# Optimization experiments

Measured on AMD Instinct MI355X. Metric: run time of the kernel, lower is better.

## Reference

```python
import jax, jax.numpy as jnp
import numpy as np

B, S, D, H = 4, 2048, 1024, 16
DK = D // H

def setup_inputs() -> dict:
    key = jax.random.key(0)
    ks = jax.random.split(key, 5)
    x = jax.random.normal(ks[0], (B, S, D), dtype=jnp.float32)
    scale = 1.0 / np.sqrt(D)
    Wq = jax.random.normal(ks[1], (D, D), dtype=jnp.float32) * scale
    Wk = jax.random.normal(ks[2], (D, D), dtype=jnp.float32) * scale
    Wv = jax.random.normal(ks[3], (D, D), dtype=jnp.float32) * scale
    Wo = jax.random.normal(ks[4], (D, D), dtype=jnp.float32) * scale
    return {"x": x, "Wq": Wq, "Wk": Wk, "Wv": Wv, "Wo": Wo}

def reference(x, Wq, Wk, Wv, Wo):
    # F.linear: y = x @ W.T  (weights stored torch-style [out, in])
    q = jnp.einsum('bsd,ed->bse', x, Wq).reshape(B, S, H, DK).transpose(0, 2, 1, 3)
    k = jnp.einsum('bsd,ed->bse', x, Wk).reshape(B, S, H, DK).transpose(0, 2, 1, 3)
    v = jnp.einsum('bsd,ed->bse', x, Wv).reshape(B, S, H, DK).transpose(0, 2, 1, 3)
    scores = jnp.einsum('bhqd,bhkd->bhqk', q, k) / jnp.sqrt(jnp.float32(DK))
    attn = jax.nn.softmax(scores, axis=-1)  # dropout p=0.0 -> identity
    out = jnp.einsum('bhqk,bhkd->bhqd', attn, v)
    out = out.transpose(0, 2, 1, 3).reshape(B, S, D)
    return jnp.einsum('bsd,ed->bse', out, Wo)
```

## Files before the change

### kernel.cpp

```cpp
#include <hip/hip_runtime.h>
#include <hip/hip_bf16.h>

#define B_ 4
#define S_ 2048
#define D_ 1024
#define H_ 16
#define DK_ 64

typedef __attribute__((ext_vector_type(8))) short short8;
typedef __attribute__((ext_vector_type(4))) float floatx4;
typedef __attribute__((ext_vector_type(16))) float floatx16;
typedef __attribute__((ext_vector_type(4))) unsigned int uint4v;

#define QSCL 0.1803368801111204f

static __device__ __forceinline__ unsigned short f2bf(float f) {
    unsigned int u = __float_as_uint(f);
    u += 0x7fffu + ((u >> 16) & 1u);
    return (unsigned short)(u >> 16);
}

static __device__ __forceinline__ unsigned int pack2bf_perm(float a, float b) {
    unsigned int u0 = __float_as_uint(a) + 0x8000u;
    unsigned int u1 = __float_as_uint(b) + 0x8000u;
    return __builtin_amdgcn_perm(u1, u0, 0x07060302u);
}

static __device__ __forceinline__ unsigned int pack2bf(float a, float b) {
    return (unsigned int)f2bf(a) | ((unsigned int)f2bf(b) << 16);
}

#define PLSWAP(a, b) asm volatile("v_permlane32_swap_b32 %0, %1" : "+v"(a), "+v"(b))

struct CastAll {
    const float* x;
    const float* w[4];
    unsigned short* xd;
    unsigned short* wd[4];
};

__global__ void cast_all_kernel(CastAll a) {
    int i = blockIdx.x * blockDim.x + threadIdx.x;
    const float* s;
    unsigned short* d;
    int j;
    if (i < 2097152) {
        s = a.x; d = a.xd; j = i;
    } else {
        int k = i - 2097152;
        int w = k >> 18;
        j = k & 262143;
        s = a.w[w]; d = a.wd[w];
    }
    float4 v = ((const float4*)s)[j];
    ushort4 o;
    o.x = f2bf(v.x); o.y = f2bf(v.y); o.z = f2bf(v.z); o.w = f2bf(v.w);
    ((ushort4*)d)[j] = o;
}

template <typename OutT, bool VT2>
__global__ __launch_bounds__(256) void gemm_bt(
    const unsigned short* __restrict__ A,
    const unsigned short* __restrict__ W0,
    const unsigned short* __restrict__ W1,
    const unsigned short* __restrict__ W2,
    OutT* __restrict__ C0, OutT* __restrict__ C1, OutT* __restrict__ C2,
    int M, int N, int K)
{
    __shared__ __align__(16) unsigned short At[128 * 64];
    __shared__ __align__(16) unsigned short Bt[128 * 64];

    const unsigned short* W = (blockIdx.z == 0) ? W0 : ((blockIdx.z == 1) ? W1 : W2);
    OutT* C = (blockIdx.z == 0) ? C0 : ((blockIdx.z == 1) ? C1 : C2);

    const int n0 = blockIdx.x * 128;
    const int m0 = blockIdx.y * 128;
    const int wv = threadIdx.x >> 6;
    const int ln = threadIdx.x & 63;
    const int l31 = ln & 31;
    const int half = ln >> 5;
    const int wm = (wv >> 1) * 64;
    const int wn = (wv & 1) * 64;

    floatx16 acc[2][2];
#pragma unroll
    for (int mt = 0; mt < 2; mt++)
#pragma unroll
        for (int nt = 0; nt < 2; nt++)
#pragma unroll
            for (int e = 0; e < 16; e++) acc[mt][nt][e] = 0.f;

    const int lr = ln >> 3;
    const int lc = (((ln & 7) ^ lr) * 8);
    const int sw = (l31 & 7);

    for (int k0 = 0; k0 < K; k0 += 64) {
        __syncthreads();
#pragma unroll
        for (int c = 0; c < 4; c++) {
            int rowA = wv * 32 + c * 8;
            const unsigned short* gA = A + (size_t)(m0 + rowA + lr) * K + k0 + lc;
            __builtin_amdgcn_global_load_lds(
                (const __attribute__((address_space(1))) void*)gA,
                (__attribute__((address_space(3))) void*)&At[rowA * 64], 16, 0, 0);
            const unsigned short* gB = W + (size_t)(n0 + rowA + lr) * K + k0 + lc;
            __builtin_amdgcn_global_load_lds(
                (const __attribute__((address_space(1))) void*)gB,
                (__attribute__((address_space(3))) void*)&Bt[rowA * 64], 16, 0, 0);
        }
        __syncthreads();

#pragma unroll
        for (int ks = 0; ks < 4; ks++) {
            const int slot = ((ks * 2 + half) ^ sw) * 8;
            short8 af[2], bf[2];
#pragma unroll
            for (int mt = 0; mt < 2; mt++)
                af[mt] = *(const short8*)&At[(wm + mt * 32 + l31) * 64 + slot];
#pragma unroll
            for (int nt = 0; nt < 2; nt++)
                bf[nt] = *(const short8*)&Bt[(wn + nt * 32 + l31) * 64 + slot];
#pragma unroll
            for (int mt = 0; mt < 2; mt++)
#pragma unroll
                for (int nt = 0; nt < 2; nt++)
                    acc[mt][nt] = __builtin_amdgcn_mfma_f32_32x32x16_bf16(af[mt], bf[nt], acc[mt][nt], 0, 0, 0);
        }
    }

    const float esc = (VT2 && blockIdx.z == 0) ? QSCL : 1.0f;

    if constexpr (VT2) {
        if (blockIdx.z == 2) {
            unsigned short* Vt = (unsigned short*)C;
#pragma unroll
            for (int mt = 0; mt < 2; mt++)
#pragma unroll
                for (int nt = 0; nt < 2; nt++)
#pragma unroll
                    for (int rg = 0; rg < 4; rg++) {
                        int col = n0 + wn + nt * 32 + l31;
                        int row0 = m0 + wm + mt * 32 + 4 * half + 8 * rg;
                        int bb = row0 >> 11, ss = row0 & 2047;
                        size_t addr = ((size_t)(bb * 1024 + col)) * 2048 + ss;
                        uint2 pk;
                        pk.x = pack2bf(acc[mt][nt][4 * rg + 0], acc[mt][nt][4 * rg + 1]);
                        pk.y = pack2bf(acc[mt][nt][4 * rg + 2], acc[mt][nt][4 * rg + 3]);
                        *(uint2*)(Vt + addr) = pk;
                    }
            return;
        }
    }

#pragma unroll
    for (int mt = 0; mt < 2; mt++)
#pragma unroll
        for (int nt = 0; nt < 2; nt++)
#pragma unroll
            for (int rg = 0; rg < 4; rg++)
#pragma unroll
                for (int r = 0; r < 4; r++) {
                    int row = m0 + wm + mt * 32 + 4 * half + 8 * rg + r;
                    int col = n0 + wn + nt * 32 + l31;
                    float v = acc[mt][nt][4 * rg + r] * esc;
                    if constexpr (sizeof(OutT) == 2)
                        C[(size_t)row * N + col] = (OutT)f2bf(v);
                    else
                        C[(size_t)row * N + col] = v;
                }
}

__global__ __launch_bounds__(256, 2) void flash_attn(
    const unsigned short* __restrict__ Q,
    const unsigned short* __restrict__ K,
    const unsigned short* __restrict__ Vt,
    unsigned short* __restrict__ O)
{
    __shared__ __align__(16) unsigned short Kt[2][64 * 72];
    __shared__ __align__(16) unsigned short VT[2][64 * 72];

    const int qt = blockIdx.x;
    const int h = blockIdx.y;
    const int b = blockIdx.z;
    const int tid = threadIdx.x;
    const int wv = tid >> 6;
    const int ln = tid & 63;
    const int l31 = ln & 31;
    const int half = ln >> 5;

    const size_t base = ((size_t)b * S_) * D_ + (size_t)h * DK_;
    const size_t vtbase = ((size_t)(b * 1024 + h * 64)) * (size_t)S_;

    const int qrow0 = qt * 256 + wv * 64 + l31;
    short8 qf[2][4];
#pragma unroll
    for (int qh = 0; qh < 2; qh++) {
        const unsigned short* qp = Q + base + (size_t)(qrow0 + qh * 32) * D_ + half * 8;
#pragma unroll
        for (int ks = 0; ks < 4; ks++) qf[qh][ks] = *(const short8*)(qp + ks * 16);
    }

    floatx16 Oacc[2][2];
#pragma unroll
    for (int qh = 0; qh < 2; qh++)
#pragma unroll
        for (int mt = 0; mt < 2; mt++)
#pragma unroll
            for (int e = 0; e < 16; e++) Oacc[qh][mt][e] = 0.f;
    float l_i[2] = {0.f, 0.f};

    const int srow = tid >> 3;
    const int scol = (tid & 7) * 8;
    const unsigned short* kp0 = K + base + (size_t)srow * D_ + scol;
    const unsigned short* kp1 = kp0 + (size_t)32 * D_;
    const unsigned short* vp0 = Vt + vtbase + (size_t)srow * S_ + scol;
    const unsigned short* vp1 = vp0 + (size_t)32 * S_;
    const int swo = srow * 72 + scol;

    short8 kr0 = *(const short8*)kp0;
    short8 kr1 = *(const short8*)kp1;
    short8 vr0 = *(const short8*)vp0;
    short8 vr1 = *(const short8*)vp1;
    kp0 += (size_t)64 * D_; kp1 += (size_t)64 * D_;
    vp0 += 64; vp1 += 64;

    for (int kt = 0; kt < S_ / 64; kt++) {
        const int cb = kt & 1;
        unsigned short* Kc = &Kt[cb][0];
        unsigned short* Vc = &VT[cb][0];
        *(short8*)&Kc[swo] = kr0;
        *(short8*)&Kc[swo + 32 * 72] = kr1;
        *(short8*)&Vc[swo] = vr0;
        *(short8*)&Vc[swo + 32 * 72] = vr1;
        __syncthreads();

        if (kt < S_ / 64 - 1) {
            kr0 = *(const short8*)kp0;
            kr1 = *(const short8*)kp1;
            vr0 = *(const short8*)vp0;
            vr1 = *(const short8*)vp1;
            kp0 += (size_t)64 * D_; kp1 += (size_t)64 * D_;
            vp0 += 64; vp1 += 64;
        }

        uint2 run[2][2][4];

#pragma unroll
        for (int mt = 0; mt < 2; mt++) {
            floatx16 sac[2];
#pragma unroll
            for (int qh = 0; qh < 2; qh++)
#pragma unroll
                for (int e = 0; e < 16; e++) sac[qh][e] = 0.f;
            __builtin_amdgcn_s_setprio(1);
#pragma unroll
            for (int ks = 0; ks < 4; ks++) {
                short8 kf = *(const short8*)&Kc[(mt * 32 + l31) * 72 + ks * 16 + half * 8];
                sac[0] = __builtin_amdgcn_mfma_f32_32x32x16_bf16(kf, qf[0][ks], sac[0], 0, 0, 0);
                sac[1] = __builtin_amdgcn_mfma_f32_32x32x16_bf16(kf, qf[1][ks], sac[1], 0, 0, 0);
            }
            __builtin_amdgcn_s_setprio(0);
#pragma unroll
            for (int qh = 0; qh < 2; qh++)
#pragma unroll
                for (int g = 0; g < 4; g++) {
                    float p0 = __builtin_amdgcn_exp2f(sac[qh][4 * g + 0]);
                    float p1 = __builtin_amdgcn_exp2f(sac[qh][4 * g + 1]);
                    float p2 = __builtin_amdgcn_exp2f(sac[qh][4 * g + 2]);
                    float p3 = __builtin_amdgcn_exp2f(sac[qh][4 * g + 3]);
                    l_i[qh] += (p0 + p1) + (p2 + p3);
                    run[qh][mt][g].x = pack2bf_perm(p0, p1);
                    run[qh][mt][g].y = pack2bf_perm(p2, p3);
                }
        }

#pragma unroll
        for (int qh = 0; qh < 2; qh++)
#pragma unroll
            for (int mt = 0; mt < 2; mt++)
#pragma unroll
                for (int t = 0; t < 2; t++) {
                    PLSWAP(run[qh][mt][2 * t].x, run[qh][mt][2 * t + 1].x);
                    PLSWAP(run[qh][mt][2 * t].y, run[qh][mt][2 * t + 1].y);
                }

#pragma unroll
        for (int mt2 = 0; mt2 < 2; mt2++)
#pragma unroll
            for (int t = 0; t < 2; t++) {
                int ks = mt2 * 2 + t;
                short8 pf[2];
#pragma unroll
                for (int qh = 0; qh < 2; qh++) {
                    uint4v u = {run[qh][mt2][2 * t].x, run[qh][mt2][2 * t].y,
                                run[qh][mt2][2 * t + 1].x, run[qh][mt2][2 * t + 1].y};
                    pf[qh] = __builtin_bit_cast(short8, u);
                }
                __builtin_amdgcn_s_setprio(1);
#pragma unroll
                for (int mt = 0; mt < 2; mt++) {
                    short8 vf = *(const short8*)&Vc[(mt * 32 + l31) * 72 + ks * 16 + half * 8];
                    Oacc[0][mt] = __builtin_amdgcn_mfma_f32_32x32x16_bf16(vf, pf[0], Oacc[0][mt], 0, 0, 0);
                    Oacc[1][mt] = __builtin_amdgcn_mfma_f32_32x32x16_bf16(vf, pf[1], Oacc[1][mt], 0, 0, 0);
                }
                __builtin_amdgcn_s_setprio(0);
            }
    }

#pragma unroll
    for (int qh = 0; qh < 2; qh++) {
        float ls = l_i[qh] + __shfl_xor(l_i[qh], 32);
        float inv = 1.0f / ls;
        const size_t orow = base + (size_t)(qrow0 + qh * 32) * D_;
#pragma unroll
        for (int mt = 0; mt < 2; mt++)
#pragma unroll
            for (int g = 0; g < 4; g++) {
                uint2 pk;
                pk.x = pack2bf(Oacc[qh][mt][4 * g + 0] * inv, Oacc[qh][mt][4 * g + 1] * inv);
                pk.y = pack2bf(Oacc[qh][mt][4 * g + 2] * inv, Oacc[qh][mt][4 * g + 3] * inv);
                *(uint2*)(O + orow + mt * 32 + 8 * g + 4 * half) = pk;
            }
    }
}

extern "C" void kernel_launch(void* const* d_in, const int* in_sizes, int n_in,
                              void* d_out, int out_size, void* d_ws, size_t ws_size,
                              hipStream_t stream) {
    const float* x  = (const float*)d_in[0];
    const float* Wq = (const float*)d_in[1];
    const float* Wk = (const float*)d_in[2];
    const float* Wv = (const float*)d_in[3];
    const float* Wo = (const float*)d_in[4];
    float* out = (float*)d_out;

    char* ws = (char*)d_ws;
    const size_t MB = 1024 * 1024;
    unsigned short* xb  = (unsigned short*)(ws);
    unsigned short* wqb = (unsigned short*)(ws + 16 * MB);
    unsigned short* wkb = (unsigned short*)(ws + 18 * MB);
    unsigned short* wvb = (unsigned short*)(ws + 20 * MB);
    unsigned short* wob = (unsigned short*)(ws + 22 * MB);
    unsigned short* Qb  = (unsigned short*)(ws + 24 * MB);
    unsigned short* Kb  = (unsigned short*)(ws + 40 * MB);
    unsigned short* Vtb = (unsigned short*)(ws + 56 * MB);
    unsigned short* Ob  = (unsigned short*)(ws);

    CastAll ca;
    ca.x = x; ca.xd = xb;
    ca.w[0] = Wq; ca.w[1] = Wk; ca.w[2] = Wv; ca.w[3] = Wo;
    ca.wd[0] = wqb; ca.wd[1] = wkb; ca.wd[2] = wvb; ca.wd[3] = wob;
    cast_all_kernel<<<12288, 256, 0, stream>>>(ca);

    dim3 gq(D_ / 128, (B_ * S_) / 128, 3);
    gemm_bt<unsigned short, true><<<gq, 256, 0, stream>>>(
        xb, wqb, wkb, wvb, Qb, Kb, Vtb, B_ * S_, D_, D_);

    dim3 gf(S_ / 256, H_, B_);
    flash_attn<<<gf, 256, 0, stream>>>(Qb, Kb, Vtb, Ob);

    dim3 go(D_ / 128, (B_ * S_) / 128, 1);
    gemm_bt<float, false><<<go, 256, 0, stream>>>(
        Ob, wob, wob, wob, out, out, out, B_ * S_, D_, D_);
}
```

Before: 283.8 us.

## Use 512-thread flash blocks with one 32-row query tile per wave

After: 273.0 us. 1.04x faster.

```diff
diff --git a/kernel.cpp b/kernel.cpp
--- a/kernel.cpp
+++ b/kernel.cpp
@@ -170,7 +170,7 @@
                 }
 }
 
-__global__ __launch_bounds__(256, 2) void flash_attn(
+__global__ __launch_bounds__(512, 4) void flash_attn(
     const unsigned short* __restrict__ Q,
     const unsigned short* __restrict__ K,
     const unsigned short* __restrict__ Vt,
@@ -179,9 +179,10 @@
     __shared__ __align__(16) unsigned short Kt[2][64 * 72];
     __shared__ __align__(16) unsigned short VT[2][64 * 72];
 
-    const int qt = blockIdx.x;
-    const int h = blockIdx.y;
-    const int b = blockIdx.z;
+    const int pair = blockIdx.x;
+    const int h = pair & 15;
+    const int b = pair >> 4;
+    const int qt = blockIdx.y;
     const int tid = threadIdx.x;
     const int wv = tid >> 6;
     const int ln = tid & 63;
@@ -191,134 +192,110 @@
     const size_t base = ((size_t)b * S_) * D_ + (size_t)h * DK_;
     const size_t vtbase = ((size_t)(b * 1024 + h * 64)) * (size_t)S_;
 
-    const int qrow0 = qt * 256 + wv * 64 + l31;
-    short8 qf[2][4];
-#pragma unroll
-    for (int qh = 0; qh < 2; qh++) {
-        const unsigned short* qp = Q + base + (size_t)(qrow0 + qh * 32) * D_ + half * 8;
-#pragma unroll
-        for (int ks = 0; ks < 4; ks++) qf[qh][ks] = *(const short8*)(qp + ks * 16);
-    }
-
-    floatx16 Oacc[2][2];
-#pragma unroll
-    for (int qh = 0; qh < 2; qh++)
-#pragma unroll
-        for (int mt = 0; mt < 2; mt++)
-#pragma unroll
-            for (int e = 0; e < 16; e++) Oacc[qh][mt][e] = 0.f;
-    float l_i[2] = {0.f, 0.f};
+    const int qrow = qt * 256 + wv * 32 + l31;
+    short8 qf[4];
+    {
+        const unsigned short* qp = Q + base + (size_t)qrow * D_ + half * 8;
+#pragma unroll
+        for (int ks = 0; ks < 4; ks++) qf[ks] = *(const short8*)(qp + ks * 16);
+    }
+
+    floatx16 Oacc[2];
+#pragma unroll
+    for (int mt = 0; mt < 2; mt++)
+#pragma unroll
+        for (int e = 0; e < 16; e++) Oacc[mt][e] = 0.f;
+    float l_i = 0.f;
 
     const int srow = tid >> 3;
     const int scol = (tid & 7) * 8;
-    const unsigned short* kp0 = K + base + (size_t)srow * D_ + scol;
-    const unsigned short* kp1 = kp0 + (size_t)32 * D_;
-    const unsigned short* vp0 = Vt + vtbase + (size_t)srow * S_ + scol;
-    const unsigned short* vp1 = vp0 + (size_t)32 * S_;
+    const unsigned short* kp = K + base + (size_t)srow * D_ + scol;
+    const unsigned short* vp = Vt + vtbase + (size_t)srow * S_ + scol;
     const int swo = srow * 72 + scol;
 
-    short8 kr0 = *(const short8*)kp0;
-    short8 kr1 = *(const short8*)kp1;
-    short8 vr0 = *(const short8*)vp0;
-    short8 vr1 = *(const short8*)vp1;
-    kp0 += (size_t)64 * D_; kp1 += (size_t)64 * D_;
-    vp0 += 64; vp1 += 64;
+    short8 kr = *(const short8*)kp;
+    short8 vr = *(const short8*)vp;
+    kp += (size_t)64 * D_;
+    vp += 64;
 
     for (int kt = 0; kt < S_ / 64; kt++) {
         const int cb = kt & 1;
         unsigned short* Kc = &Kt[cb][0];
         unsigned short* Vc = &VT[cb][0];
-        *(short8*)&Kc[swo] = kr0;
-        *(short8*)&Kc[swo + 32 * 72] = kr1;
-        *(short8*)&Vc[swo] = vr0;
-        *(short8*)&Vc[swo + 32 * 72] = vr1;
+        *(short8*)&Kc[swo] = kr;
+        *(short8*)&Vc[swo] = vr;
         __syncthreads();
 
         if (kt < S_ / 64 - 1) {
-            kr0 = *(const short8*)kp0;
-            kr1 = *(const short8*)kp1;
-            vr0 = *(const short8*)vp0;
-            vr1 = *(const short8*)vp1;
-            kp0 += (size_t)64 * D_; kp1 += (size_t)64 * D_;
-            vp0 += 64; vp1 += 64;
-        }
-
-        uint2 run[2][2][4];
+            kr = *(const short8*)kp;
+            vr = *(const short8*)vp;
+            kp += (size_t)64 * D_;
+            vp += 64;
+        }
+
+        uint2 run[2][4];
 
 #pragma unroll
         for (int mt = 0; mt < 2; mt++) {
-            floatx16 sac[2];
-#pragma unroll
-            for (int qh = 0; qh < 2; qh++)
-#pragma unroll
-                for (int e = 0; e < 16; e++) sac[qh][e] = 0.f;
+            floatx16 sac;
+#pragma unroll
+            for (int e = 0; e < 16; e++) sac[e] = 0.f;
             __builtin_amdgcn_s_setprio(1);
 #pragma unroll
             for (int ks = 0; ks < 4; ks++) {
                 short8 kf = *(const short8*)&Kc[(mt * 32 + l31) * 72 + ks * 16 + half * 8];
-                sac[0] = __builtin_amdgcn_mfma_f32_32x32x16_bf16(kf, qf[0][ks], sac[0], 0, 0, 0);
-                sac[1] = __builtin_amdgcn_mfma_f32_32x32x16_bf16(kf, qf[1][ks], sac[1], 0, 0, 0);
+                sac = __builtin_amdgcn_mfma_f32_32x32x16_bf16(kf, qf[ks], sac, 0, 0, 0);
             }
             __builtin_amdgcn_s_setprio(0);
 #pragma unroll
-            for (int qh = 0; qh < 2; qh++)
-#pragma unroll
-                for (int g = 0; g < 4; g++) {
-                    float p0 = __builtin_amdgcn_exp2f(sac[qh][4 * g + 0]);
-                    float p1 = __builtin_amdgcn_exp2f(sac[qh][4 * g + 1]);
-                    float p2 = __builtin_amdgcn_exp2f(sac[qh][4 * g + 2]);
-                    float p3 = __builtin_amdgcn_exp2f(sac[qh][4 * g + 3]);
-                    l_i[qh] += (p0 + p1) + (p2 + p3);
-                    run[qh][mt][g].x = pack2bf_perm(p0, p1);
-                    run[qh][mt][g].y = pack2bf_perm(p2, p3);
-                }
-        }
-
-#pragma unroll
-        for (int qh = 0; qh < 2; qh++)
-#pragma unroll
-            for (int mt = 0; mt < 2; mt++)
-#pragma unroll
-                for (int t = 0; t < 2; t++) {
-                    PLSWAP(run[qh][mt][2 * t].x, run[qh][mt][2 * t + 1].x);
-                    PLSWAP(run[qh][mt][2 * t].y, run[qh][mt][2 * t + 1].y);
-                }
+            for (int g = 0; g < 4; g++) {
+                float p0 = __builtin_amdgcn_exp2f(sac[4 * g + 0]);
+                float p1 = __builtin_amdgcn_exp2f(sac[4 * g + 1]);
+                float p2 = __builtin_amdgcn_exp2f(sac[4 * g + 2]);
+                float p3 = __builtin_amdgcn_exp2f(sac[4 * g + 3]);
+                l_i += (p0 + p1) + (p2 + p3);
+                run[mt][g].x = pack2bf_perm(p0, p1);
+                run[mt][g].y = pack2bf_perm(p2, p3);
+            }
+        }
+
+#pragma unroll
+        for (int mt = 0; mt < 2; mt++)
+#pragma unroll
+            for (int t = 0; t < 2; t++) {
+                PLSWAP(run[mt][2 * t].x, run[mt][2 * t + 1].x);
+                PLSWAP(run[mt][2 * t].y, run[mt][2 * t + 1].y);
+            }
 
 #pragma unroll
         for (int mt2 = 0; mt2 < 2; mt2++)
 #pragma unroll
             for (int t = 0; t < 2; t++) {
                 int ks = mt2 * 2 + t;
-                short8 pf[2];
-#pragma unroll
-                for (int qh = 0; qh < 2; qh++) {
-                    uint4v u = {run[qh][mt2][2 * t].x, run[qh][mt2][2 * t].y,
-                                run[qh][mt2][2 * t + 1].x, run[qh][mt2][2 * t + 1].y};
-                    pf[qh] = __builtin_bit_cast(short8, u);
-                }
+                uint4v u = {run[mt2][2 * t].x, run[mt2][2 * t].y,
+                            run[mt2][2 * t + 1].x, run[mt2][2 * t + 1].y};
+                short8 pf = __builtin_bit_cast(short8, u);
                 __builtin_amdgcn_s_setprio(1);
 #pragma unroll
                 for (int mt = 0; mt < 2; mt++) {
                     short8 vf = *(const short8*)&Vc[(mt * 32 + l31) * 72 + ks * 16 + half * 8];
-                    Oacc[0][mt] = __builtin_amdgcn_mfma_f32_32x32x16_bf16(vf, pf[0], Oacc[0][mt], 0, 0, 0);
-                    Oacc[1][mt] = __builtin_amdgcn_mfma_f32_32x32x16_bf16(vf, pf[1], Oacc[1][mt], 0, 0, 0);
+                    Oacc[mt] = __builtin_amdgcn_mfma_f32_32x32x16_bf16(vf, pf, Oacc[mt], 0, 0, 0);
                 }
                 __builtin_amdgcn_s_setprio(0);
             }
     }
 
-#pragma unroll
-    for (int qh = 0; qh < 2; qh++) {
-        float ls = l_i[qh] + __shfl_xor(l_i[qh], 32);
+    {
+        float ls = l_i + __shfl_xor(l_i, 32);
         float inv = 1.0f / ls;
-        const size_t orow = base + (size_t)(qrow0 + qh * 32) * D_;
+        const size_t orow = base + (size_t)qrow * D_;
 #pragma unroll
         for (int mt = 0; mt < 2; mt++)
 #pragma unroll
             for (int g = 0; g < 4; g++) {
                 uint2 pk;
-                pk.x = pack2bf(Oacc[qh][mt][4 * g + 0] * inv, Oacc[qh][mt][4 * g + 1] * inv);
-                pk.y = pack2bf(Oacc[qh][mt][4 * g + 2] * inv, Oacc[qh][mt][4 * g + 3] * inv);
+                pk.x = pack2bf(Oacc[mt][4 * g + 0] * inv, Oacc[mt][4 * g + 1] * inv);
+                pk.y = pack2bf(Oacc[mt][4 * g + 2] * inv, Oacc[mt][4 * g + 3] * inv);
                 *(uint2*)(O + orow + mt * 32 + 8 * g + 4 * half) = pk;
             }
     }
@@ -356,8 +333,8 @@
     gemm_bt<unsigned short, true><<<gq, 256, 0, stream>>>(
         xb, wqb, wkb, wvb, Qb, Kb, Vtb, B_ * S_, D_, D_);
 
-    dim3 gf(S_ / 256, H_, B_);
-    flash_attn<<<gf, 256, 0, stream>>>(Qb, Kb, Vtb, Ob);
+    dim3 gf(64, S_ / 256, 1);
+    flash_attn<<<gf, 512, 0, stream>>>(Qb, Kb, Vtb, Ob);
 
     dim3 go(D_ / 128, (B_ * S_) / 128, 1);
     gemm_bt<float, false><<<go, 256, 0, stream>>>(
```
